# Optimization experiments

Measured on AMD Instinct MI355X. Metric: run time of the kernel, lower is better.

## Reference

```python
import jax, jax.numpy as jnp
import numpy as np

D_MODEL = 1024
NUM_HEADS = 16
D_K = D_MODEL // NUM_HEADS  # 64
THETA = 10000.0
MAX_SEQ_LEN = 2048


def _trunc_normal(key, shape, std):
    # approximate trunc_normal_(mean=0, std, a=-3*std, b=3*std)
    u = jax.random.truncated_normal(key, -3.0, 3.0, shape, dtype=jnp.float32)
    return u * std


def setup_inputs() -> dict:
    key = jax.random.key(0)
    ks = jax.random.split(key, 5)
    x = jax.random.normal(ks[0], (2, 2048, D_MODEL), dtype=jnp.float32)
    token_positions = jnp.arange(2048, dtype=jnp.int64 if jax.config.jax_enable_x64 else jnp.int32)
    sigma = 2.0 / (D_MODEL + D_MODEL)
    Wq = _trunc_normal(ks[1], (D_MODEL, D_MODEL), sigma)
    Wk = _trunc_normal(ks[2], (D_MODEL, D_MODEL), sigma)
    Wv = _trunc_normal(ks[3], (D_MODEL, D_MODEL), sigma)
    Wo = _trunc_normal(ks[4], (D_MODEL, D_MODEL), sigma)
    return {"in_features": x, "Wq": Wq, "Wk": Wk, "Wv": Wv, "Wo": Wo,
            "token_positions": token_positions}


def _rope(x, cos_phi, sin_phi):
    # x: (..., seq, d_k); cos/sin: (seq, d_k//2)
    x_even = x[..., 0::2]
    x_odd = x[..., 1::2]
    y_even = x_even * cos_phi - x_odd * sin_phi
    y_odd = x_even * sin_phi + x_odd * cos_phi
    # interleave back
    y = jnp.stack([y_even, y_odd], axis=-1)
    return y.reshape(x.shape)


def reference(in_features, Wq, Wk, Wv, Wo, token_positions):
    b, s, d = in_features.shape
    h, dk = NUM_HEADS, D_K
    # projections: weight is (d_out, d_in)
    q = jnp.einsum('bsd,ed->bse', in_features, Wq)
    k = jnp.einsum('bsd,ed->bse', in_features, Wk)
    v = jnp.einsum('bsd,ed->bse', in_features, Wv)
    # split heads: (b, h, s, dk)
    q = q.reshape(b, s, h, dk).transpose(0, 2, 1, 3)
    k = k.reshape(b, s, h, dk).transpose(0, 2, 1, 3)
    v = v.reshape(b, s, h, dk).transpose(0, 2, 1, 3)
    # RoPE tables
    inv_freq = 1.0 / (THETA ** (jnp.arange(0, dk, 2, dtype=jnp.float32) / dk))
    phi = token_positions.astype(jnp.float32)[:, None] * inv_freq[None, :]  # (s, dk/2)
    cos_phi, sin_phi = jnp.cos(phi), jnp.sin(phi)
    q = _rope(q, cos_phi, sin_phi)
    k = _rope(k, cos_phi, sin_phi)
    # causal mask
    mask = jnp.tril(jnp.ones((s, s), dtype=bool))
    scores = jnp.einsum('bhqd,bhkd->bhqk', q, k) / jnp.sqrt(jnp.float32(dk))
    scores = jnp.where(mask, scores, -jnp.inf)
    attn = jax.nn.softmax(scores, axis=-1)
    out = jnp.einsum('bhqk,bhkd->bhqd', attn, v)
    out = out.transpose(0, 2, 1, 3).reshape(b, s, d)
    return jnp.einsum('bsd,ed->bse', out, Wo)
```

## Files before the change

### kernel.cpp

```cpp
#include <hip/hip_runtime.h>
#include <hip/hip_bf16.h>
#include <math.h>

#define S_  2048
#define DM_ 1024

typedef unsigned short u16;
typedef __attribute__((ext_vector_type(8))) short short8;
typedef __attribute__((ext_vector_type(4))) float f32x4;

__device__ __forceinline__ u16 f2bf(float f) {
  unsigned u = __float_as_uint(f);
  u += 0x7fffu + ((u >> 16) & 1u);
  return (u16)(u >> 16);
}
__device__ __forceinline__ float bf2f(u16 h) {
  return __uint_as_float((unsigned)h << 16);
}
__device__ __forceinline__ unsigned pack_bf2(float a, float b) {
  union { __hip_bfloat162 h2; unsigned u; } cv;
  cv.h2 = __float22bfloat162_rn(float2{a, b});
  return cv.u;
}
__device__ __forceinline__ void cp16(const void* g, void* l) {
  __builtin_amdgcn_global_load_lds(
      (const __attribute__((address_space(1))) unsigned*)(uintptr_t)g,
      (__attribute__((address_space(3))) unsigned*)(unsigned)(uintptr_t)l, 16, 0, 0);
}

struct CastArgs { const float* src[5]; u16* dst[5]; int n[5]; };

__global__ __launch_bounds__(256) void cast_kernel(CastArgs a) {
  const int z = blockIdx.y;
  const int i = (blockIdx.x * 256 + threadIdx.x) * 8;
  if (i >= a.n[z]) return;
  const float4* s = (const float4*)(a.src[z] + i);
  float4 v0 = s[0], v1 = s[1];
  short8 r;
  r[0] = (short)f2bf(v0.x); r[1] = (short)f2bf(v0.y);
  r[2] = (short)f2bf(v0.z); r[3] = (short)f2bf(v0.w);
  r[4] = (short)f2bf(v1.x); r[5] = (short)f2bf(v1.y);
  r[6] = (short)f2bf(v1.z); r[7] = (short)f2bf(v1.w);
  *(short8*)(a.dst[z] + i) = r;
}

struct GemmArgs { const u16* A; const u16* W[3]; void* out[3]; int modes; };

#define SLOT_BYTES 49152
#define NKT 16

__global__ __launch_bounds__(512, 2) void gemm_mfma(GemmArgs g) {
  __shared__ __align__(16) char lds[3 * SLOT_BYTES];
  const int tid = threadIdx.x, lane = tid & 63, w = tid >> 6;
  const int wm = w >> 1, wn = w & 1;
  const int t = lane & 15, u = lane >> 4;
  const int l3 = lane >> 3, l7 = lane & 7;
  const int z = blockIdx.z;
  const int m0 = blockIdx.y * 256, n0 = blockIdx.x * 128;
  const u16* __restrict__ A = g.A;
  const u16* __restrict__ W = g.W[z];

  const int axor = l7 << 4;
  const int ksw = (l7 ^ l3) * 8;
  const u16* Ab = A + (size_t)(m0 + w * 8 + l3) * 1024 + ksw;
  const u16* Wb = W + (size_t)(n0 + w * 8 + l3) * 1024 + ksw;
  char* const ldsw = lds + w * 1024;

  auto stg = [&](int kt, int slot, int r0, int r1) {
    char* sb = ldsw + slot * SLOT_BYTES;
    #pragma unroll
    for (int r = r0; r <= r1; r++) {
      if (r < 4) cp16(Ab + (size_t)r * 65536 + kt * 64, sb + r * 8192);
      else       cp16(Wb + (size_t)(r - 4) * 65536 + kt * 64, sb + 32768 + (r - 4) * 8192);
    }
  };

  const f32x4 fz = {0.f, 0.f, 0.f, 0.f};
  f32x4 acc[4][4];
  #pragma unroll
  for (int i = 0; i < 4; i++)
    #pragma unroll
    for (int j = 0; j < 4; j++) acc[i][j] = fz;

  stg(0, 0, 0, 5);
  stg(1, 1, 0, 5);
  asm volatile("s_waitcnt vmcnt(6)" ::: "memory");
  __builtin_amdgcn_s_barrier();

  int sc = 0;
  for (int kt = 0; kt < NKT; kt++) {
    const char* cs = lds + sc * SLOT_BYTES;
    int sp = sc + 2; if (sp >= 3) sp -= 3;
    const bool pf = (kt + 2 < NKT);

    #pragma unroll
    for (int ks = 0; ks < 2; ks++) {
      short8 af[4], bfr[4];
      const int co = (ks * 64 + u * 16) ^ axor;
      const char* ap = cs + (wm * 64 + t) * 128 + co;
      const char* bp = cs + 32768 + (wn * 64 + t) * 128 + co;
      #pragma unroll
      for (int mf = 0; mf < 4; mf++) af[mf] = *(const short8*)(ap + mf * 2048);
      #pragma unroll
      for (int nf = 0; nf < 4; nf++) bfr[nf] = *(const short8*)(bp + nf * 2048);
      if (pf) stg(kt + 2, sp, ks * 3, ks * 3 + 2);

      __builtin_amdgcn_s_barrier();
      asm volatile("s_waitcnt lgkmcnt(0)" ::: "memory");
      __builtin_amdgcn_sched_barrier(0);
      __builtin_amdgcn_s_setprio(1);
      #pragma unroll
      for (int mf = 0; mf < 4; mf++)
        #pragma unroll
        for (int nf = 0; nf < 4; nf++)
          acc[mf][nf] = __builtin_amdgcn_mfma_f32_16x16x32_bf16(af[mf], bfr[nf], acc[mf][nf], 0, 0, 0);
      __builtin_amdgcn_s_setprio(0);
      if (ks == 1) {
        if (pf)                { asm volatile("s_waitcnt vmcnt(6)" ::: "memory"); }
        else if (kt + 1 < NKT) { asm volatile("s_waitcnt vmcnt(0)" ::: "memory"); }
      }
      __builtin_amdgcn_s_barrier();
    }
    sc++; if (sc == 3) sc = 0;
  }

  const int mode = (g.modes >> (2 * z)) & 3;
  const int rbase = m0 + wm * 64 + u * 4;
  const int cbase = n0 + wn * 64 + t;
  if (mode == 0) {
    u16* O = (u16*)g.out[z];
    #pragma unroll
    for (int mt = 0; mt < 4; mt++)
      #pragma unroll
      for (int nt = 0; nt < 4; nt++)
        #pragma unroll
        for (int r = 0; r < 4; r++)
          O[(size_t)(rbase + mt * 16 + r) * 1024 + cbase + nt * 16] = f2bf(acc[mt][nt][r]);
  } else if (mode == 1) {
    u16* O = (u16*)g.out[z];
    #pragma unroll
    for (int mt = 0; mt < 4; mt++)
      #pragma unroll
      for (int nt = 0; nt < 4; nt++) {
        int gr = rbase + mt * 16;
        int b = gr >> 11, s0 = gr & (S_ - 1);
        int gc = cbase + nt * 16;
        int h = gc >> 6, d = gc & 63;
        ushort4 v;
        v.x = f2bf(acc[mt][nt][0]); v.y = f2bf(acc[mt][nt][1]);
        v.z = f2bf(acc[mt][nt][2]); v.w = f2bf(acc[mt][nt][3]);
        *(ushort4*)&O[(size_t)((b * 16 + h) * 64 + d) * 2048 + s0] = v;
      }
  } else {
    float* O = (float*)g.out[z];
    #pragma unroll
    for (int mt = 0; mt < 4; mt++)
      #pragma unroll
      for (int nt = 0; nt < 4; nt++)
        #pragma unroll
        for (int r = 0; r < 4; r++)
          O[(size_t)(rbase + mt * 16 + r) * 1024 + cbase + nt * 16] = acc[mt][nt][r];
  }
}

__global__ __launch_bounds__(256) void rope_kernel(u16* qb, u16* kb, const int* __restrict__ tp) {
  const int isq = (blockIdx.y == 0);
  u16* p = isq ? qb : kb;
  const float outscale = isq ? 0.18033688011112042f : 1.0f;
  const int i = (blockIdx.x * 256 + threadIdx.x) * 8;
  const int s = (i >> 10) & (S_ - 1);
  const int d = i & 63;
  const float pos = (float)tp[s];
  short8 v = *(short8*)(p + i);
  #pragma unroll
  for (int j = 0; j < 4; j++) {
    float inv = exp2f(-(float)(d + 2 * j) * 0.20762050593046439f);
    float phi = pos * inv;
    float sn, cs;
    sincosf(phi, &sn, &cs);
    float xe = bf2f((u16)v[2 * j]), xo = bf2f((u16)v[2 * j + 1]);
    v[2 * j]     = (short)f2bf((xe * cs - xo * sn) * outscale);
    v[2 * j + 1] = (short)f2bf((xe * sn + xo * cs) * outscale);
  }
  *(short8*)(p + i) = v;
}

__global__ __launch_bounds__(512, 4) void attn_mfma(const u16* __restrict__ qb, const u16* __restrict__ kb,
                                                    const u16* __restrict__ vt, u16* __restrict__ ab) {
  __shared__ __align__(16) u16 Qs[2][4096];
  __shared__ __align__(16) u16 Ks[2][4096];
  __shared__ __align__(16) u16 Vs[2][4096];

  const int tid = threadIdx.x, lane = tid & 63, w = tid >> 6;
  const int v = w & 3, g = w >> 2;
  const int t = lane & 15, u = lane >> 4;
  const int bh = blockIdx.y, b = bh >> 4, h = bh & 15;
  const int i = blockIdx.x;
  const int qa = 31 - i;
  const int qbt = i;
  const int nk = 32 - i;
  const size_t qkb = (size_t)b * S_ * 1024 + h * 64;
  const size_t vtb = (size_t)bh * 64 * 2048;

  {
    const int qtile = g ? qbt : qa;
    cp16(qb + qkb + (size_t)(qtile * 64 + lane) * 1024 + v * 8,       (char*)Qs[g] + v * 1024);
    cp16(qb + qkb + (size_t)(qtile * 64 + lane) * 1024 + (v + 4) * 8, (char*)Qs[g] + 4096 + v * 1024);
  }
  cp16(kb + qkb + (size_t)lane * 1024 + w * 8, (char*)Ks[0] + w * 1024);
  cp16(vt + vtb + (size_t)lane * 2048 + w * 8, (char*)Vs[0] + w * 1024);
  __syncthreads();

  short8 aqA[2], aqP[2];
  #pragma unroll
  for (int ks = 0; ks < 2; ks++) {
    aqA[ks] = *(const short8*)((const char*)Qs[0] + (ks * 4 + u) * 1024 + (v * 16 + t) * 16);
    short8 bq = *(const short8*)((const char*)Qs[1] + (ks * 4 + u) * 1024 + (v * 16 + t) * 16);
    aqP[ks] = g ? bq : aqA[ks];
  }

  const f32x4 fzero = {0.f, 0.f, 0.f, 0.f};
  f32x4 oPrim[4], oSec[4];
  #pragma unroll
  for (int ct = 0; ct < 4; ct++) { oPrim[ct] = fzero; oSec[ct] = fzero; }
  float rsumP = 0.f, rsumS = 0.f;

  const int qprim = g ? qbt : qa;
  const int qrowP = qprim * 64 + v * 16 + t;
  const int qrowA = qa * 64 + v * 16 + t;

  for (int kt = 0; kt < nk; kt++) {
    const int cur = kt & 1, nxt = cur ^ 1;
    if (kt + 1 < nk) {
      cp16(kb + qkb + (size_t)((kt + 1) * 64 + lane) * 1024 + w * 8, (char*)Ks[nxt] + w * 1024);
      cp16(vt + vtb + (size_t)lane * 2048 + (kt + 1) * 64 + w * 8,   (char*)Vs[nxt] + w * 1024);
    }

    if (kt <= qbt) {
      f32x4 st[4] = {fzero, fzero, fzero, fzero};
      #pragma unroll
      for (int ks = 0; ks < 2; ks++)
        #pragma unroll
        for (int ct = 0; ct < 4; ct++) {
          short8 kf = *(const short8*)((const char*)Ks[cur] + (ks * 4 + u) * 1024 + (ct * 16 + t) * 16);
          st[ct] = __builtin_amdgcn_mfma_f32_16x16x32_bf16(kf, aqP[ks], st[ct], 0, 0, 0);
        }

      unsigned pb2[4][2];
      const bool diag = (kt == qprim);
      #pragma unroll
      for (int ct = 0; ct < 4; ct++) {
        float p[4];
        #pragma unroll
        for (int r = 0; r < 4; r++) {
          int key = kt * 64 + ct * 16 + 4 * u + r;
          float pv = exp2f(st[ct][r]);
          p[r] = (diag && key > qrowP) ? 0.f : pv;
          rsumP += p[r];
        }
        pb2[ct][0] = pack_bf2(p[0], p[1]);
        pb2[ct][1] = pack_bf2(p[2], p[3]);
      }

      #pragma unroll
      for (int ks = 0; ks < 2; ks++) {
        union { short8 s8; int i4[4]; } pf;
        #pragma unroll
        for (int jj = 0; jj < 4; jj++) {
          int src = 32 * (u & 1) + 16 * (jj >> 1) + t;
          int v0 = __shfl((int)pb2[ks * 2][jj & 1], src, 64);
          int v1 = __shfl((int)pb2[ks * 2 + 1][jj & 1], src, 64);
          pf.i4[jj] = (u >> 1) ? v1 : v0;
        }
        #pragma unroll
        for (int ct = 0; ct < 4; ct++) {
          short8 vf = *(const short8*)((const char*)Vs[cur] + (ks * 4 + u) * 1024 + (ct * 16 + t) * 16);
          oPrim[ct] = __builtin_amdgcn_mfma_f32_16x16x32_bf16(vf, pf.s8, oPrim[ct], 0, 0, 0);
        }
      }
    } else {
      f32x4 st2[2] = {fzero, fzero};
      #pragma unroll
      for (int ks = 0; ks < 2; ks++)
        #pragma unroll
        for (int c = 0; c < 2; c++) {
          short8 kf = *(const short8*)((const char*)Ks[cur] + (ks * 4 + u) * 1024 + ((2 * g + c) * 16 + t) * 16);
          st2[c] = __builtin_amdgcn_mfma_f32_16x16x32_bf16(kf, aqA[ks], st2[c], 0, 0, 0);
        }

      unsigned ph[2][2];
      float rs = 0.f;
      const bool diag = (kt == qa);
      #pragma unroll
      for (int c = 0; c < 2; c++) {
        float p[4];
        #pragma unroll
        for (int r = 0; r < 4; r++) {
          int key = kt * 64 + (2 * g + c) * 16 + 4 * u + r;
          float pv = exp2f(st2[c][r]);
          p[r] = (diag && key > qrowA) ? 0.f : pv;
          rs += p[r];
        }
        ph[c][0] = pack_bf2(p[0], p[1]);
        ph[c][1] = pack_bf2(p[2], p[3]);
      }

      union { short8 s8; int i4[4]; } pf;
      #pragma unroll
      for (int jj = 0; jj < 4; jj++) {
        int src = 32 * (u & 1) + 16 * (jj >> 1) + t;
        int v0 = __shfl((int)ph[0][jj & 1], src, 64);
        int v1 = __shfl((int)ph[1][jj & 1], src, 64);
        pf.i4[jj] = (u >> 1) ? v1 : v0;
      }
      if (g) {
        rsumS += rs;
        #pragma unroll
        for (int ct = 0; ct < 4; ct++) {
          short8 vf = *(const short8*)((const char*)Vs[cur] + (4 + u) * 1024 + (ct * 16 + t) * 16);
          oSec[ct] = __builtin_amdgcn_mfma_f32_16x16x32_bf16(vf, pf.s8, oSec[ct], 0, 0, 0);
        }
      } else {
        rsumP += rs;
        #pragma unroll
        for (int ct = 0; ct < 4; ct++) {
          short8 vf = *(const short8*)((const char*)Vs[cur] + u * 1024 + (ct * 16 + t) * 16);
          oPrim[ct] = __builtin_amdgcn_mfma_f32_16x16x32_bf16(vf, pf.s8, oPrim[ct], 0, 0, 0);
        }
      }
    }
    __syncthreads();
  }

  float* dmpO = (float*)Ks;
  float* dmpR = (float*)Vs;
  if (g) {
    #pragma unroll
    for (int ct = 0; ct < 4; ct++)
      *(f32x4*)&dmpO[(size_t)(v * 64 + lane) * 16 + ct * 4] = oSec[ct];
    dmpR[v * 64 + lane] = rsumS;
    float rs = rsumP;
    rs += __shfl_xor(rs, 16, 64);
    rs += __shfl_xor(rs, 32, 64);
    const float inv = 1.0f / rs;
    #pragma unroll
    for (int ct = 0; ct < 4; ct++) {
      ushort4 vv;
      vv.x = f2bf(oPrim[ct][0] * inv); vv.y = f2bf(oPrim[ct][1] * inv);
      vv.z = f2bf(oPrim[ct][2] * inv); vv.w = f2bf(oPrim[ct][3] * inv);
      *(ushort4*)&ab[((size_t)b * S_ + qrowP) * 1024 + h * 64 + ct * 16 + 4 * u] = vv;
    }
  }
  __syncthreads();
  if (!g) {
    #pragma unroll
    for (int ct = 0; ct < 4; ct++) {
      f32x4 add = *(const f32x4*)&dmpO[(size_t)(v * 64 + lane) * 16 + ct * 4];
      oPrim[ct] += add;
    }
    float rs = rsumP + dmpR[v * 64 + lane];
    rs += __shfl_xor(rs, 16, 64);
    rs += __shfl_xor(rs, 32, 64);
    const float inv = 1.0f / rs;
    #pragma unroll
    for (int ct = 0; ct < 4; ct++) {
      ushort4 vv;
      vv.x = f2bf(oPrim[ct][0] * inv); vv.y = f2bf(oPrim[ct][1] * inv);
      vv.z = f2bf(oPrim[ct][2] * inv); vv.w = f2bf(oPrim[ct][3] * inv);
      *(ushort4*)&ab[((size_t)b * S_ + qrowA) * 1024 + h * 64 + ct * 16 + 4 * u] = vv;
    }
  }
}

extern "C" void kernel_launch(void* const* d_in, const int* in_sizes, int n_in,
                              void* d_out, int out_size, void* d_ws, size_t ws_size,
                              hipStream_t stream) {
  const float* x  = (const float*)d_in[0];
  const float* Wq = (const float*)d_in[1];
  const float* Wk = (const float*)d_in[2];
  const float* Wv = (const float*)d_in[3];
  const float* Wo = (const float*)d_in[4];
  const int*   tp = (const int*)d_in[5];
  float* out = (float*)d_out;

  char* ws = (char*)d_ws;
  u16* xb  = (u16*)(ws);
  u16* wqb = (u16*)(ws + (8 << 20));
  u16* wkb = (u16*)(ws + (10 << 20));
  u16* wvb = (u16*)(ws + (12 << 20));
  u16* wob = (u16*)(ws + (14 << 20));
  u16* qbuf = (u16*)(ws + (16 << 20));
  u16* kbuf = (u16*)(ws + (24 << 20));
  u16* vtb  = (u16*)(ws + (32 << 20));
  u16* abuf = (u16*)(ws + (40 << 20));

  CastArgs ca;
  ca.src[0] = x;  ca.dst[0] = xb;  ca.n[0] = 2 * S_ * DM_;
  ca.src[1] = Wq; ca.dst[1] = wqb; ca.n[1] = DM_ * DM_;
  ca.src[2] = Wk; ca.dst[2] = wkb; ca.n[2] = DM_ * DM_;
  ca.src[3] = Wv; ca.dst[3] = wvb; ca.n[3] = DM_ * DM_;
  ca.src[4] = Wo; ca.dst[4] = wob; ca.n[4] = DM_ * DM_;
  cast_kernel<<<dim3(2048, 5), 256, 0, stream>>>(ca);

  GemmArgs gq;
  gq.A = xb;
  gq.W[0] = wqb; gq.W[1] = wkb; gq.W[2] = wvb;
  gq.out[0] = qbuf; gq.out[1] = kbuf; gq.out[2] = vtb;
  gq.modes = (1 << 4);
  gemm_mfma<<<dim3(8, 16, 3), 512, 0, stream>>>(gq);

  rope_kernel<<<dim3(2048, 2), 256, 0, stream>>>(qbuf, kbuf, tp);

  attn_mfma<<<dim3(16, 32), 512, 0, stream>>>(qbuf, kbuf, vtb, abuf);

  GemmArgs go;
  go.A = abuf;
  go.W[0] = wob; go.W[1] = wob; go.W[2] = wob;
  go.out[0] = out; go.out[1] = out; go.out[2] = out;
  go.modes = 2;
  gemm_mfma<<<dim3(8, 16, 1), 512, 0, stream>>>(go);
}
```

Baseline: 197.6 us.

## Retile GEMM to 128-row blocks with double buffering and XCD-aware block swizzle

After: 186.3 us. 1.06x faster.

```diff
diff --git a/kernel.cpp b/kernel.cpp
--- a/kernel.cpp
+++ b/kernel.cpp
@@ -46,93 +46,96 @@
 
 struct GemmArgs { const u16* A; const u16* W[3]; void* out[3]; int modes; };
 
-#define SLOT_BYTES 49152
-#define NKT 16
-
-__global__ __launch_bounds__(512, 2) void gemm_mfma(GemmArgs g) {
-  __shared__ __align__(16) char lds[3 * SLOT_BYTES];
+template<int BN, int MINW, int GXL>
+__global__ __launch_bounds__(256, MINW) void gemm_mfma(GemmArgs g) {
+  constexpr int BM = 128;
+  constexpr int NW = BN / 32;
+  constexpr int RBB = BN / 32;
+  constexpr int ABYTES = BM * 64 * 2;
+  constexpr int SLOT = ABYTES + BN * 64 * 2;
+  __shared__ __align__(16) char lds[2 * SLOT];
+
   const int tid = threadIdx.x, lane = tid & 63, w = tid >> 6;
   const int wm = w >> 1, wn = w & 1;
   const int t = lane & 15, u = lane >> 4;
   const int l3 = lane >> 3, l7 = lane & 7;
   const int z = blockIdx.z;
-  const int m0 = blockIdx.y * 256, n0 = blockIdx.x * 128;
+
+  const int nwg = (int)gridDim.y << GXL;
+  const int flat = (int)blockIdx.x + ((int)blockIdx.y << GXL);
+  const int swz = (flat & 7) * (nwg >> 3) + (flat >> 3);
+  const int m0 = (swz >> GXL) * BM;
+  const int n0 = (swz & ((1 << GXL) - 1)) * BN;
+
   const u16* __restrict__ A = g.A;
   const u16* __restrict__ W = g.W[z];
 
   const int axor = l7 << 4;
   const int ksw = (l7 ^ l3) * 8;
-  const u16* Ab = A + (size_t)(m0 + w * 8 + l3) * 1024 + ksw;
-  const u16* Wb = W + (size_t)(n0 + w * 8 + l3) * 1024 + ksw;
-  char* const ldsw = lds + w * 1024;
-
-  auto stg = [&](int kt, int slot, int r0, int r1) {
-    char* sb = ldsw + slot * SLOT_BYTES;
-    #pragma unroll
-    for (int r = r0; r <= r1; r++) {
-      if (r < 4) cp16(Ab + (size_t)r * 65536 + kt * 64, sb + r * 8192);
-      else       cp16(Wb + (size_t)(r - 4) * 65536 + kt * 64, sb + 32768 + (r - 4) * 8192);
-    }
+  const u16* Ab = A + (size_t)(m0 + l3) * 1024 + ksw;
+  const u16* Wb = W + (size_t)(n0 + l3) * 1024 + ksw;
+
+  auto stg = [&](int kt) {
+    char* sb = lds + (kt & 1) * SLOT;
+    #pragma unroll
+    for (int r = 0; r < 4; r++)
+      cp16(Ab + (size_t)(w * 4 + r) * 8192 + kt * 64, sb + (w * 4 + r) * 1024);
+    #pragma unroll
+    for (int r = 0; r < RBB; r++)
+      cp16(Wb + (size_t)(w * RBB + r) * 8192 + kt * 64, sb + ABYTES + (w * RBB + r) * 1024);
   };
 
   const f32x4 fz = {0.f, 0.f, 0.f, 0.f};
-  f32x4 acc[4][4];
+  f32x4 acc[4][NW];
   #pragma unroll
   for (int i = 0; i < 4; i++)
     #pragma unroll
-    for (int j = 0; j < 4; j++) acc[i][j] = fz;
-
-  stg(0, 0, 0, 5);
-  stg(1, 1, 0, 5);
-  asm volatile("s_waitcnt vmcnt(6)" ::: "memory");
+    for (int j = 0; j < NW; j++) acc[i][j] = fz;
+
+  stg(0);
+  asm volatile("s_waitcnt vmcnt(0)" ::: "memory");
   __builtin_amdgcn_s_barrier();
 
-  int sc = 0;
-  for (int kt = 0; kt < NKT; kt++) {
-    const char* cs = lds + sc * SLOT_BYTES;
-    int sp = sc + 2; if (sp >= 3) sp -= 3;
-    const bool pf = (kt + 2 < NKT);
-
+  for (int kt = 0; kt < 16; kt++) {
+    const char* cs = lds + (kt & 1) * SLOT;
+    if (kt < 15) stg(kt + 1);
+
+    short8 af[2][4], bfr[2][NW];
     #pragma unroll
     for (int ks = 0; ks < 2; ks++) {
-      short8 af[4], bfr[4];
       const int co = (ks * 64 + u * 16) ^ axor;
       const char* ap = cs + (wm * 64 + t) * 128 + co;
-      const char* bp = cs + 32768 + (wn * 64 + t) * 128 + co;
-      #pragma unroll
-      for (int mf = 0; mf < 4; mf++) af[mf] = *(const short8*)(ap + mf * 2048);
-      #pragma unroll
-      for (int nf = 0; nf < 4; nf++) bfr[nf] = *(const short8*)(bp + nf * 2048);
-      if (pf) stg(kt + 2, sp, ks * 3, ks * 3 + 2);
-
-      __builtin_amdgcn_s_barrier();
-      asm volatile("s_waitcnt lgkmcnt(0)" ::: "memory");
-      __builtin_amdgcn_sched_barrier(0);
-      __builtin_amdgcn_s_setprio(1);
+      const char* bp = cs + ABYTES + (wn * (BN / 2) + t) * 128 + co;
+      #pragma unroll
+      for (int mf = 0; mf < 4; mf++) af[ks][mf] = *(const short8*)(ap + mf * 2048);
+      #pragma unroll
+      for (int nf = 0; nf < NW; nf++) bfr[ks][nf] = *(const short8*)(bp + nf * 2048);
+    }
+    asm volatile("s_waitcnt lgkmcnt(0)" ::: "memory");
+    __builtin_amdgcn_sched_barrier(0);
+    __builtin_amdgcn_s_setprio(1);
+    #pragma unroll
+    for (int ks = 0; ks < 2; ks++)
       #pragma unroll
       for (int mf = 0; mf < 4; mf++)
         #pragma unroll
-        for (int nf = 0; nf < 4; nf++)
-          acc[mf][nf] = __builtin_amdgcn_mfma_f32_16x16x32_bf16(af[mf], bfr[nf], acc[mf][nf], 0, 0, 0);
-      __builtin_amdgcn_s_setprio(0);
-      if (ks == 1) {
-        if (pf)                { asm volatile("s_waitcnt vmcnt(6)" ::: "memory"); }
-        else if (kt + 1 < NKT) { asm volatile("s_waitcnt vmcnt(0)" ::: "memory"); }
-      }
-      __builtin_amdgcn_s_barrier();
-    }
-    sc++; if (sc == 3) sc = 0;
+        for (int nf = 0; nf < NW; nf++)
+          acc[mf][nf] = __builtin_amdgcn_mfma_f32_16x16x32_bf16(af[ks][mf], bfr[ks][nf], acc[mf][nf], 0, 0, 0);
+    __builtin_amdgcn_s_setprio(0);
+
+    asm volatile("s_waitcnt vmcnt(0)" ::: "memory");
+    __builtin_amdgcn_s_barrier();
   }
 
   const int mode = (g.modes >> (2 * z)) & 3;
   const int rbase = m0 + wm * 64 + u * 4;
-  const int cbase = n0 + wn * 64 + t;
+  const int cbase = n0 + wn * (BN / 2) + t;
   if (mode == 0) {
     u16* O = (u16*)g.out[z];
     #pragma unroll
     for (int mt = 0; mt < 4; mt++)
       #pragma unroll
-      for (int nt = 0; nt < 4; nt++)
+      for (int nt = 0; nt < NW; nt++)
         #pragma unroll
         for (int r = 0; r < 4; r++)
           O[(size_t)(rbase + mt * 16 + r) * 1024 + cbase + nt * 16] = f2bf(acc[mt][nt][r]);
@@ -141,7 +144,7 @@
     #pragma unroll
     for (int mt = 0; mt < 4; mt++)
       #pragma unroll
-      for (int nt = 0; nt < 4; nt++) {
+      for (int nt = 0; nt < NW; nt++) {
         int gr = rbase + mt * 16;
         int b = gr >> 11, s0 = gr & (S_ - 1);
         int gc = cbase + nt * 16;
@@ -156,7 +159,7 @@
     #pragma unroll
     for (int mt = 0; mt < 4; mt++)
       #pragma unroll
-      for (int nt = 0; nt < 4; nt++)
+      for (int nt = 0; nt < NW; nt++)
         #pragma unroll
         for (int r = 0; r < 4; r++)
           O[(size_t)(rbase + mt * 16 + r) * 1024 + cbase + nt * 16] = acc[mt][nt][r];
@@ -407,7 +410,7 @@
   gq.W[0] = wqb; gq.W[1] = wkb; gq.W[2] = wvb;
   gq.out[0] = qbuf; gq.out[1] = kbuf; gq.out[2] = vtb;
   gq.modes = (1 << 4);
-  gemm_mfma<<<dim3(8, 16, 3), 512, 0, stream>>>(gq);
+  gemm_mfma<128, 2, 3><<<dim3(8, 32, 3), 256, 0, stream>>>(gq);
 
   rope_kernel<<<dim3(2048, 2), 256, 0, stream>>>(qbuf, kbuf, tp);
 
@@ -418,5 +421,5 @@
   go.W[0] = wob; go.W[1] = wob; go.W[2] = wob;
   go.out[0] = out; go.out[1] = out; go.out[2] = out;
   go.modes = 2;
-  gemm_mfma<<<dim3(8, 16, 1), 512, 0, stream>>>(go);
-}
+  gemm_mfma<64, 3, 4><<<dim3(16, 32, 1), 256, 0, stream>>>(go);
+}
```
